# Kernel optimization log

Hardware: AMD Instinct MI355X
Metric: run time of the kernel (lower is better)

Reference implementation:

```python
import jax, jax.numpy as jnp
import numpy as np

EPS = 1e-5


def setup_inputs() -> dict:
    key = jax.random.key(0)
    ks = jax.random.split(key, 5)
    N, E, D, L = 10000, 160000, 512, 3
    x = jax.random.normal(ks[0], (N, D), dtype=jnp.float32)
    src = jax.random.randint(ks[1], (E,), 0, N, dtype=jnp.int64)
    dst = jax.random.randint(ks[2], (E,), 0, N, dtype=jnp.int64)
    gamma = jnp.ones((L, D), dtype=jnp.float32)
    beta = jnp.zeros((L, D), dtype=jnp.float32)
    # glorot-ish scale so ReLU stack stays well-conditioned
    W = jax.random.normal(ks[3], (L, D, D), dtype=jnp.float32) * (1.0 / np.sqrt(D))
    b = jnp.zeros((L, D), dtype=jnp.float32)
    return {"x": x, "src": src, "dst": dst, "gamma": gamma, "beta": beta, "W": W, "b": b}


def reference(x, src, dst, gamma, beta, W, b):
    N = x.shape[0]
    ones = jnp.ones(src.shape[0], dtype=x.dtype)
    # DGL GraphConv norm='both': src side uses out-degree, dst side uses in-degree
    out_deg = jnp.clip(jax.ops.segment_sum(ones, src, num_segments=N), 1.0)
    in_deg = jnp.clip(jax.ops.segment_sum(ones, dst, num_segments=N), 1.0)
    src_norm = (out_deg ** -0.5)[:, None]  # [N,1]
    dst_norm = (in_deg ** -0.5)[:, None]   # [N,1]
    n_layers = gamma.shape[0]
    for i in range(n_layers):
        # BatchNorm1d (training mode: batch mean, biased variance)
        mu = jnp.mean(x, axis=0)
        var = jnp.var(x, axis=0)
        x = (x - mu) * jax.lax.rsqrt(var + EPS) * gamma[i] + beta[i]
        h = x * src_norm
        agg = jax.ops.segment_sum(h[src], dst, num_segments=N) * dst_norm
        x = jax.nn.relu(agg @ W[i] + b[i])
    return x
```

## Files before the change

### kernel.cpp

```cpp
#include <hip/hip_runtime.h>
#include <hip/hip_bf16.h>

constexpr int N = 10000;
constexpr int D = 512;
constexpr int E = 160000;
constexpr int L = 3;
constexpr float EPS = 1e-5f;

typedef _Float16 half8 __attribute__((ext_vector_type(8)));
typedef _Float16 half2v __attribute__((ext_vector_type(2)));
typedef float floatx4 __attribute__((ext_vector_type(4)));

__device__ __forceinline__ void glds16(const _Float16* g, _Float16* l) {
    __builtin_amdgcn_global_load_lds(
        (const __attribute__((address_space(1))) uint32_t*)(g),
        (__attribute__((address_space(3))) uint32_t*)(l),
        16, 0, 0);
}

constexpr int DEG_BLOCKS  = (E + 255) / 256;
constexpr int CONV_BLOCKS = 100;
constexpr int TW_BLOCKS   = L * 256;
constexpr int MEGA_BLOCKS = DEG_BLOCKS + CONV_BLOCKS + TW_BLOCKS;

__global__ __launch_bounds__(256) void mega_setup(
    const int* __restrict__ src, const int* __restrict__ dst,
    const float* __restrict__ x, const float* __restrict__ W,
    int* __restrict__ out_deg, int* __restrict__ in_deg,
    _Float16* __restrict__ x16, float* __restrict__ stats0,
    _Float16* __restrict__ Wt) {
    __shared__ float tb[32][33];
    int bid = blockIdx.x;
    int tid = threadIdx.x;
    if (bid < DEG_BLOCKS) {
        int e = bid * 256 + tid;
        if (e < E) {
            atomicAdd(&out_deg[src[e]], 1);
            atomicAdd(&in_deg[dst[e]], 1);
        }
    } else if (bid < DEG_BLOCKS + CONV_BLOCKS) {
        int b = bid - DEG_BLOCKS;
        int r0 = b * 100;
        int r1 = r0 + 100; if (r1 > N) r1 = N;
        int c2 = tid * 2;
        float s0 = 0.f, s1 = 0.f, q0 = 0.f, q1 = 0.f;
        for (int r = r0; r < r1; ++r) {
            float2 v = *(const float2*)(x + (size_t)r * D + c2);
            s0 += v.x; q0 += v.x * v.x;
            s1 += v.y; q1 += v.y * v.y;
            half2v h; h[0] = (_Float16)v.x; h[1] = (_Float16)v.y;
            *(half2v*)(x16 + (size_t)r * D + c2) = h;
        }
        atomicAdd(&stats0[c2], s0);
        atomicAdd(&stats0[c2 + 1], s1);
        atomicAdd(&stats0[D + c2], q0);
        atomicAdd(&stats0[D + c2 + 1], q1);
    } else {
        int b = bid - DEG_BLOCKS - CONV_BLOCKS;
        int l = b >> 8;
        int t = b & 255;
        int k0 = (t >> 4) * 32, n0 = (t & 15) * 32;
        int tx = tid & 31, ty = tid >> 5;
        const float* Wl = W + (size_t)l * D * D;
        _Float16* Wtl = Wt + (size_t)l * D * D;
        for (int i = 0; i < 32; i += 8)
            tb[ty + i][tx] = Wl[(size_t)(k0 + ty + i) * D + n0 + tx];
        __syncthreads();
        for (int i = 0; i < 32; i += 8)
            Wtl[(size_t)(n0 + ty + i) * D + k0 + tx] = (_Float16)tb[tx][ty + i];
    }
}

__global__ void scan_indeg(const int* __restrict__ in_deg,
                           const int* __restrict__ out_deg,
                           int* __restrict__ off, int* __restrict__ cursor,
                           float* __restrict__ src_norm, float* __restrict__ dst_norm) {
    __shared__ int lsum[1024];
    int t = threadIdx.x;
    const int chunk = (N + 1023) / 1024;
    int start = t * chunk;
    int end = start + chunk; if (end > N) end = N;
    int s = 0;
    for (int i = start; i < end; ++i) s += in_deg[i];
    lsum[t] = s;
    __syncthreads();
    for (int d = 1; d < 1024; d <<= 1) {
        int v = (t >= d) ? lsum[t - d] : 0;
        __syncthreads();
        lsum[t] += v;
        __syncthreads();
    }
    int excl = (t == 0) ? 0 : lsum[t - 1];
    for (int i = start; i < end; ++i) {
        off[i] = excl;
        cursor[i] = excl;
        excl += in_deg[i];
        int od = out_deg[i]; if (od < 1) od = 1;
        int id = in_deg[i];  if (id < 1) id = 1;
        src_norm[i] = rsqrtf((float)od);
        dst_norm[i] = rsqrtf((float)id);
    }
    if (t == 1023) off[N] = lsum[1023];
}

__global__ void csr_fill(const int* __restrict__ src, const int* __restrict__ dst,
                         int* __restrict__ cursor, int* __restrict__ csr_src) {
    int e = blockIdx.x * blockDim.x + threadIdx.x;
    if (e >= E) return;
    int d = dst[e];
    int pos = atomicAdd(&cursor[d], 1);
    csr_src[pos] = src[e];
}

__global__ __launch_bounds__(256) void aggregate_bn(
    const _Float16* __restrict__ x, const int* __restrict__ off,
    const int* __restrict__ csr_src, const float* __restrict__ src_norm,
    const float* __restrict__ dst_norm, const float* __restrict__ stats,
    const float* __restrict__ gamma, const float* __restrict__ beta,
    _Float16* __restrict__ agg) {
    int wid = (blockIdx.x * 256 + threadIdx.x) >> 6;
    if (wid >= N) return;
    int lane = threadIdx.x & 63;
    int c0 = lane * 8;

    float scale[8], shift[8];
    const float invN = 1.0f / (float)N;
    for (int i = 0; i < 8; ++i) {
        int c = c0 + i;
        float mu = stats[c] * invN;
        float var = stats[D + c] * invN - mu * mu;
        float sc = gamma[c] * rsqrtf(var + EPS);
        scale[i] = sc;
        shift[i] = beta[c] - mu * sc;
    }

    int e0 = off[wid], e1 = off[wid + 1];
    float a[8] = {}, a2[8] = {};
    float t = 0.f;
    int e = e0;
    for (; e + 4 <= e1; e += 4) {
        int s0 = csr_src[e];
        int s1 = csr_src[e + 1];
        int s2 = csr_src[e + 2];
        int s3 = csr_src[e + 3];
        float n0 = src_norm[s0];
        float n1 = src_norm[s1];
        float n2 = src_norm[s2];
        float n3 = src_norm[s3];
        half8 v0 = *(const half8*)(x + (size_t)s0 * D + c0);
        half8 v1 = *(const half8*)(x + (size_t)s1 * D + c0);
        half8 v2 = *(const half8*)(x + (size_t)s2 * D + c0);
        half8 v3 = *(const half8*)(x + (size_t)s3 * D + c0);
        t += (n0 + n1) + (n2 + n3);
        for (int k = 0; k < 8; ++k) {
            a[k]  += (float)v0[k] * n0;
            a2[k] += (float)v1[k] * n1;
            a[k]  += (float)v2[k] * n2;
            a2[k] += (float)v3[k] * n3;
        }
    }
    for (; e < e1; ++e) {
        int s0 = csr_src[e];
        float n0 = src_norm[s0];
        half8 v0 = *(const half8*)(x + (size_t)s0 * D + c0);
        t += n0;
        for (int k = 0; k < 8; ++k) a[k] += (float)v0[k] * n0;
    }
    float dn = dst_norm[wid];
    half8 o;
    for (int i = 0; i < 8; ++i)
        o[i] = (_Float16)(dn * (scale[i] * (a[i] + a2[i]) + shift[i] * t));
    *(half8*)(agg + (size_t)wid * D + c0) = o;
}

template <typename OutT, bool STATS>
__global__ __launch_bounds__(256) void mm_f16_relu(
    const _Float16* __restrict__ A, const _Float16* __restrict__ Bt,
    const float* __restrict__ bias, OutT* __restrict__ C, int M,
    float* __restrict__ stats) {
    __shared__ __align__(16) _Float16 As[128 * 32];
    __shared__ __align__(16) _Float16 Bs[128 * 32];
    const int tid  = threadIdx.x;
    const int wave = tid >> 6;
    const int lane = tid & 63;
    const int quad = lane >> 4;
    const int l16  = lane & 15;
    const int row0 = blockIdx.x * 128;
    const int col0 = blockIdx.y * 128;
    const int wm = (wave & 1) * 64;
    const int wn = (wave >> 1) * 64;
    const int sr = lane >> 2;
    const int sc = (lane & 3) * 8;

    int ar0 = row0 + wave * 32 + sr;
    int ar1 = ar0 + 16;
    if (ar0 >= M) ar0 = M - 1;
    if (ar1 >= M) ar1 = M - 1;
    const _Float16* gA0 = A + (size_t)ar0 * D + sc;
    const _Float16* gA1 = A + (size_t)ar1 * D + sc;
    const _Float16* gB0 = Bt + (size_t)(col0 + wave * 32 + sr) * D + sc;
    const _Float16* gB1 = Bt + (size_t)(col0 + wave * 32 + 16 + sr) * D + sc;
    _Float16* lA0 = As + (wave * 32) * 32;
    _Float16* lA1 = As + (wave * 32 + 16) * 32;
    _Float16* lB0 = Bs + (wave * 32) * 32;
    _Float16* lB1 = Bs + (wave * 32 + 16) * 32;

    floatx4 acc[4][4] = {};

    for (int k0 = 0; k0 < D; k0 += 32) {
        __syncthreads();
        glds16(gA0 + k0, lA0);
        glds16(gA1 + k0, lA1);
        glds16(gB0 + k0, lB0);
        glds16(gB1 + k0, lB1);
        __syncthreads();
        half8 af[4], bf[4];
        for (int i = 0; i < 4; ++i)
            af[i] = *(const half8*)(As + (wm + i * 16 + l16) * 32 + quad * 8);
        for (int j = 0; j < 4; ++j)
            bf[j] = *(const half8*)(Bs + (wn + j * 16 + l16) * 32 + quad * 8);
        for (int i = 0; i < 4; ++i)
            for (int j = 0; j < 4; ++j)
                acc[i][j] = __builtin_amdgcn_mfma_f32_16x16x32_f16(
                    af[i], bf[j], acc[i][j], 0, 0, 0);
    }

    float s[4] = {}, q[4] = {};
    for (int i = 0; i < 4; ++i) {
        for (int r = 0; r < 4; ++r) {
            int row = row0 + wm + i * 16 + quad * 4 + r;
            bool valid = row < M;
            for (int j = 0; j < 4; ++j) {
                int col = col0 + wn + j * 16 + l16;
                float v = acc[i][j][r] + bias[col];
                v = v > 0.f ? v : 0.f;
                if (valid) {
                    C[(size_t)row * D + col] = (OutT)v;
                    if (STATS) { s[j] += v; q[j] += v * v; }
                }
            }
        }
    }
    if (STATS) {
        for (int j = 0; j < 4; ++j) {
            float sv = s[j], qv = q[j];
            sv += __shfl_xor(sv, 16); sv += __shfl_xor(sv, 32);
            qv += __shfl_xor(qv, 16); qv += __shfl_xor(qv, 32);
            if (quad == 0) {
                int col = col0 + wn + j * 16 + l16;
                atomicAdd(&stats[col], sv);
                atomicAdd(&stats[D + col], qv);
            }
        }
    }
}

extern "C" void kernel_launch(void* const* d_in, const int* in_sizes, int n_in,
                              void* d_out, int out_size, void* d_ws, size_t ws_size,
                              hipStream_t stream) {
    const float* x_in  = (const float*)d_in[0];
    const int*   src   = (const int*)d_in[1];
    const int*   dst   = (const int*)d_in[2];
    const float* gamma = (const float*)d_in[3];
    const float* beta  = (const float*)d_in[4];
    const float* W     = (const float*)d_in[5];
    const float* b     = (const float*)d_in[6];
    float* out = (float*)d_out;

    char* p = (char*)d_ws;
    _Float16* x16 = (_Float16*)p;  p += (size_t)N * D * 2;
    _Float16* agg = (_Float16*)p;  p += (size_t)N * D * 2;
    _Float16* Wt  = (_Float16*)p;  p += (size_t)L * D * D * 2;
    float* src_norm = (float*)p;   p += (size_t)N * 4;
    float* dst_norm = (float*)p;   p += (size_t)N * 4;
    int* out_deg   = (int*)p;      p += (size_t)N * 4;
    int* in_deg    = (int*)p;      p += (size_t)N * 4;
    float* stats0  = (float*)p;    p += 2 * D * 4;
    float* stats1  = (float*)p;    p += 2 * D * 4;
    float* stats2  = (float*)p;    p += 2 * D * 4;
    int* csr_off   = (int*)p;      p += (size_t)(N + 1) * 4;
    int* cursor    = (int*)p;      p += (size_t)N * 4;
    int* csr_src   = (int*)p;      p += (size_t)E * 4;

    float* stats_in[3] = {stats0, stats1, stats2};

    hipMemsetAsync(out_deg, 0, (2 * (size_t)N + 6 * D) * sizeof(int), stream);
    mega_setup<<<MEGA_BLOCKS, 256, 0, stream>>>(src, dst, x_in, W,
                                                out_deg, in_deg, x16, stats0, Wt);
    scan_indeg<<<1, 1024, 0, stream>>>(in_deg, out_deg, csr_off, cursor,
                                       src_norm, dst_norm);
    csr_fill<<<DEG_BLOCKS, 256, 0, stream>>>(src, dst, cursor, csr_src);

    dim3 mm_grid((N + 127) / 128, D / 128);
    const int agg_blocks = (N + 3) / 4;

    for (int l = 0; l < L; ++l) {
        const float* gl  = gamma + (size_t)l * D;
        const float* bl  = beta + (size_t)l * D;
        const _Float16* Wl = Wt + (size_t)l * D * D;
        const float* bil = b + (size_t)l * D;

        aggregate_bn<<<agg_blocks, 256, 0, stream>>>(
            x16, csr_off, csr_src, src_norm, dst_norm, stats_in[l], gl, bl, agg);
        if (l == L - 1) {
            mm_f16_relu<float, false><<<mm_grid, 256, 0, stream>>>(
                agg, Wl, bil, out, N, nullptr);
        } else {
            mm_f16_relu<_Float16, true><<<mm_grid, 256, 0, stream>>>(
                agg, Wl, bil, x16, N, stats_in[l + 1]);
        }
    }
}
```

Baseline: 282.3 us.

## Prescale features by src_norm, precompute per-dst norm sums, shard aggregation across column slices

Node features are now stored already multiplied by src_norm: the initial conversion does this in a new combined CSR-fill/convert kernel, and the GEMM epilogue does it for later layers. The per-destination sum of src_norm is accumulated once into T during CSR fill. This removes the per-edge src_norm gathers and multiplies from every layer's aggregation. Aggregation is split into 4 column shards per node, with four edge groups per wave reduced by shuffles, to raise parallelism and memory-level concurrency. The cost is extra atomics on T, more blocks, shuffle reductions, and an additional fp16 rounding of the prescaled values.

```diff
diff --git a/kernel.cpp b/kernel.cpp
--- a/kernel.cpp
+++ b/kernel.cpp
@@ -7,6 +7,9 @@
 constexpr int L = 3;
 constexpr float EPS = 1e-5f;
 
+constexpr int NSH = 4;
+constexpr int SHC = D / NSH;
+
 typedef _Float16 half8 __attribute__((ext_vector_type(8)));
 typedef _Float16 half2v __attribute__((ext_vector_type(2)));
 typedef float floatx4 __attribute__((ext_vector_type(4)));
@@ -19,16 +22,15 @@
 }
 
 constexpr int DEG_BLOCKS  = (E + 255) / 256;
-constexpr int CONV_BLOCKS = 100;
+constexpr int STAT_BLOCKS = 500;
 constexpr int TW_BLOCKS   = L * 256;
-constexpr int MEGA_BLOCKS = DEG_BLOCKS + CONV_BLOCKS + TW_BLOCKS;
+constexpr int MEGA_BLOCKS = DEG_BLOCKS + STAT_BLOCKS + TW_BLOCKS;
 
 __global__ __launch_bounds__(256) void mega_setup(
     const int* __restrict__ src, const int* __restrict__ dst,
     const float* __restrict__ x, const float* __restrict__ W,
     int* __restrict__ out_deg, int* __restrict__ in_deg,
-    _Float16* __restrict__ x16, float* __restrict__ stats0,
-    _Float16* __restrict__ Wt) {
+    float* __restrict__ stats0, _Float16* __restrict__ Wt) {
     __shared__ float tb[32][33];
     int bid = blockIdx.x;
     int tid = threadIdx.x;
@@ -38,25 +40,23 @@
             atomicAdd(&out_deg[src[e]], 1);
             atomicAdd(&in_deg[dst[e]], 1);
         }
-    } else if (bid < DEG_BLOCKS + CONV_BLOCKS) {
+    } else if (bid < DEG_BLOCKS + STAT_BLOCKS) {
         int b = bid - DEG_BLOCKS;
-        int r0 = b * 100;
-        int r1 = r0 + 100; if (r1 > N) r1 = N;
+        int r0 = b * 20;
+        int r1 = r0 + 20; if (r1 > N) r1 = N;
         int c2 = tid * 2;
         float s0 = 0.f, s1 = 0.f, q0 = 0.f, q1 = 0.f;
         for (int r = r0; r < r1; ++r) {
             float2 v = *(const float2*)(x + (size_t)r * D + c2);
             s0 += v.x; q0 += v.x * v.x;
             s1 += v.y; q1 += v.y * v.y;
-            half2v h; h[0] = (_Float16)v.x; h[1] = (_Float16)v.y;
-            *(half2v*)(x16 + (size_t)r * D + c2) = h;
         }
         atomicAdd(&stats0[c2], s0);
         atomicAdd(&stats0[c2 + 1], s1);
         atomicAdd(&stats0[D + c2], q0);
         atomicAdd(&stats0[D + c2 + 1], q1);
     } else {
-        int b = bid - DEG_BLOCKS - CONV_BLOCKS;
+        int b = bid - DEG_BLOCKS - STAT_BLOCKS;
         int l = b >> 8;
         int t = b & 255;
         int k0 = (t >> 4) * 32, n0 = (t & 15) * 32;
@@ -103,81 +103,98 @@
     if (t == 1023) off[N] = lsum[1023];
 }
 
-__global__ void csr_fill(const int* __restrict__ src, const int* __restrict__ dst,
-                         int* __restrict__ cursor, int* __restrict__ csr_src) {
-    int e = blockIdx.x * blockDim.x + threadIdx.x;
-    if (e >= E) return;
-    int d = dst[e];
-    int pos = atomicAdd(&cursor[d], 1);
-    csr_src[pos] = src[e];
-}
-
-__global__ __launch_bounds__(256) void aggregate_bn(
-    const _Float16* __restrict__ x, const int* __restrict__ off,
-    const int* __restrict__ csr_src, const float* __restrict__ src_norm,
+constexpr int CONV_BLOCKS = 500;
+__global__ __launch_bounds__(256) void csr_fill_conv(
+    const int* __restrict__ src, const int* __restrict__ dst,
+    const float* __restrict__ x, const float* __restrict__ src_norm,
+    int* __restrict__ cursor, int* __restrict__ csr_src,
+    float* __restrict__ T, _Float16* __restrict__ x16) {
+    int bid = blockIdx.x;
+    int tid = threadIdx.x;
+    if (bid < DEG_BLOCKS) {
+        int e = bid * 256 + tid;
+        if (e < E) {
+            int s = src[e], d = dst[e];
+            int pos = atomicAdd(&cursor[d], 1);
+            csr_src[pos] = s;
+            atomicAdd(&T[d], src_norm[s]);
+        }
+    } else {
+        int b = bid - DEG_BLOCKS;
+        int r0 = b * 20;
+        int r1 = r0 + 20; if (r1 > N) r1 = N;
+        int c2 = tid * 2;
+        for (int r = r0; r < r1; ++r) {
+            float sn = src_norm[r];
+            float2 v = *(const float2*)(x + (size_t)r * D + c2);
+            half2v h;
+            h[0] = (_Float16)(v.x * sn);
+            h[1] = (_Float16)(v.y * sn);
+            *(half2v*)(x16 + (size_t)r * D + c2) = h;
+        }
+    }
+}
+
+__global__ __launch_bounds__(256) void aggregate4(
+    const _Float16* __restrict__ xs, const int* __restrict__ off,
+    const int* __restrict__ csr_src, const float* __restrict__ T,
     const float* __restrict__ dst_norm, const float* __restrict__ stats,
     const float* __restrict__ gamma, const float* __restrict__ beta,
     _Float16* __restrict__ agg) {
-    int wid = (blockIdx.x * 256 + threadIdx.x) >> 6;
-    if (wid >= N) return;
+    int shard = blockIdx.x & 3;
+    int wid = (blockIdx.x >> 2) * 4 + (threadIdx.x >> 6);
     int lane = threadIdx.x & 63;
-    int c0 = lane * 8;
-
-    float scale[8], shift[8];
-    const float invN = 1.0f / (float)N;
-    for (int i = 0; i < 8; ++i) {
-        int c = c0 + i;
-        float mu = stats[c] * invN;
-        float var = stats[D + c] * invN - mu * mu;
-        float sc = gamma[c] * rsqrtf(var + EPS);
-        scale[i] = sc;
-        shift[i] = beta[c] - mu * sc;
-    }
+    int eg = lane >> 4;
+    int ch = lane & 15;
+    int c0 = shard * SHC + ch * 8;
 
     int e0 = off[wid], e1 = off[wid + 1];
-    float a[8] = {}, a2[8] = {};
-    float t = 0.f;
-    int e = e0;
-    for (; e + 4 <= e1; e += 4) {
+    const _Float16* xp = xs + c0;
+    float a[8] = {}, b2[8] = {};
+    int e = e0 + eg;
+    for (; e + 4 < e1; e += 8) {
         int s0 = csr_src[e];
-        int s1 = csr_src[e + 1];
-        int s2 = csr_src[e + 2];
-        int s3 = csr_src[e + 3];
-        float n0 = src_norm[s0];
-        float n1 = src_norm[s1];
-        float n2 = src_norm[s2];
-        float n3 = src_norm[s3];
-        half8 v0 = *(const half8*)(x + (size_t)s0 * D + c0);
-        half8 v1 = *(const half8*)(x + (size_t)s1 * D + c0);
-        half8 v2 = *(const half8*)(x + (size_t)s2 * D + c0);
-        half8 v3 = *(const half8*)(x + (size_t)s3 * D + c0);
-        t += (n0 + n1) + (n2 + n3);
+        int s1 = csr_src[e + 4];
+        half8 v0 = *(const half8*)(xp + (size_t)s0 * D);
+        half8 v1 = *(const half8*)(xp + (size_t)s1 * D);
+#pragma unroll
+        for (int k = 0; k < 8; ++k) { a[k] += (float)v0[k]; b2[k] += (float)v1[k]; }
+    }
+    if (e < e1) {
+        int s0 = csr_src[e];
+        half8 v0 = *(const half8*)(xp + (size_t)s0 * D);
+#pragma unroll
+        for (int k = 0; k < 8; ++k) a[k] += (float)v0[k];
+    }
+#pragma unroll
+    for (int k = 0; k < 8; ++k) {
+        a[k] += b2[k];
+        a[k] += __shfl_xor(a[k], 16);
+        a[k] += __shfl_xor(a[k], 32);
+    }
+    if (eg == 0) {
+        float t = T[wid];
+        float dn = dst_norm[wid];
+        const float invN = 1.0f / (float)N;
+        half8 o;
+#pragma unroll
         for (int k = 0; k < 8; ++k) {
-            a[k]  += (float)v0[k] * n0;
-            a2[k] += (float)v1[k] * n1;
-            a[k]  += (float)v2[k] * n2;
-            a2[k] += (float)v3[k] * n3;
-        }
-    }
-    for (; e < e1; ++e) {
-        int s0 = csr_src[e];
-        float n0 = src_norm[s0];
-        half8 v0 = *(const half8*)(x + (size_t)s0 * D + c0);
-        t += n0;
-        for (int k = 0; k < 8; ++k) a[k] += (float)v0[k] * n0;
-    }
-    float dn = dst_norm[wid];
-    half8 o;
-    for (int i = 0; i < 8; ++i)
-        o[i] = (_Float16)(dn * (scale[i] * (a[i] + a2[i]) + shift[i] * t));
-    *(half8*)(agg + (size_t)wid * D + c0) = o;
+            int c = c0 + k;
+            float mu = stats[c] * invN;
+            float var = stats[D + c] * invN - mu * mu;
+            float sc = gamma[c] * rsqrtf(var + EPS);
+            float sh = beta[c] - mu * sc;
+            o[k] = (_Float16)(dn * (sc * a[k] + sh * t));
+        }
+        *(half8*)(agg + (size_t)wid * D + c0) = o;
+    }
 }
 
 template <typename OutT, bool STATS>
 __global__ __launch_bounds__(256) void mm_f16_relu(
     const _Float16* __restrict__ A, const _Float16* __restrict__ Bt,
     const float* __restrict__ bias, OutT* __restrict__ C, int M,
-    float* __restrict__ stats) {
+    float* __restrict__ stats, const float* __restrict__ src_norm) {
     __shared__ __align__(16) _Float16 As[128 * 32];
     __shared__ __align__(16) _Float16 Bs[128 * 32];
     const int tid  = threadIdx.x;
@@ -230,13 +247,19 @@
         for (int r = 0; r < 4; ++r) {
             int row = row0 + wm + i * 16 + quad * 4 + r;
             bool valid = row < M;
+            float sn = 1.0f;
+            if (STATS && valid) sn = src_norm[row];
             for (int j = 0; j < 4; ++j) {
                 int col = col0 + wn + j * 16 + l16;
                 float v = acc[i][j][r] + bias[col];
                 v = v > 0.f ? v : 0.f;
                 if (valid) {
-                    C[(size_t)row * D + col] = (OutT)v;
-                    if (STATS) { s[j] += v; q[j] += v * v; }
+                    if (STATS) {
+                        C[(size_t)row * D + col] = (OutT)(v * sn);
+                        s[j] += v; q[j] += v * v;
+                    } else {
+                        C[(size_t)row * D + col] = (OutT)v;
+                    }
                 }
             }
         }
@@ -278,21 +301,23 @@
     float* stats0  = (float*)p;    p += 2 * D * 4;
     float* stats1  = (float*)p;    p += 2 * D * 4;
     float* stats2  = (float*)p;    p += 2 * D * 4;
+    float* T       = (float*)p;    p += (size_t)N * 4;
     int* csr_off   = (int*)p;      p += (size_t)(N + 1) * 4;
     int* cursor    = (int*)p;      p += (size_t)N * 4;
     int* csr_src   = (int*)p;      p += (size_t)E * 4;
 
     float* stats_in[3] = {stats0, stats1, stats2};
 
-    hipMemsetAsync(out_deg, 0, (2 * (size_t)N + 6 * D) * sizeof(int), stream);
+    hipMemsetAsync(out_deg, 0, (3 * (size_t)N + 6 * D) * sizeof(int), stream);
     mega_setup<<<MEGA_BLOCKS, 256, 0, stream>>>(src, dst, x_in, W,
-                                                out_deg, in_deg, x16, stats0, Wt);
+                                                out_deg, in_deg, stats0, Wt);
     scan_indeg<<<1, 1024, 0, stream>>>(in_deg, out_deg, csr_off, cursor,
                                        src_norm, dst_norm);
-    csr_fill<<<DEG_BLOCKS, 256, 0, stream>>>(src, dst, cursor, csr_src);
+    csr_fill_conv<<<DEG_BLOCKS + CONV_BLOCKS, 256, 0, stream>>>(
+        src, dst, x_in, src_norm, cursor, csr_src, T, x16);
 
     dim3 mm_grid((N + 127) / 128, D / 128);
-    const int agg_blocks = (N + 3) / 4;
+    const int agg_blocks = NSH * ((N + 3) / 4);
 
     for (int l = 0; l < L; ++l) {
         const float* gl  = gamma + (size_t)l * D;
@@ -300,14 +325,14 @@
         const _Float16* Wl = Wt + (size_t)l * D * D;
         const float* bil = b + (size_t)l * D;
 
-        aggregate_bn<<<agg_blocks, 256, 0, stream>>>(
-            x16, csr_off, csr_src, src_norm, dst_norm, stats_in[l], gl, bl, agg);
+        aggregate4<<<agg_blocks, 256, 0, stream>>>(
+            x16, csr_off, csr_src, T, dst_norm, stats_in[l], gl, bl, agg);
         if (l == L - 1) {
             mm_f16_relu<float, false><<<mm_grid, 256, 0, stream>>>(
-                agg, Wl, bil, out, N, nullptr);
+                agg, Wl, bil, out, N, nullptr, nullptr);
         } else {
             mm_f16_relu<_Float16, true><<<mm_grid, 256, 0, stream>>>(
-                agg, Wl, bil, x16, N, stats_in[l + 1]);
-        }
-    }
-}
+                agg, Wl, bil, x16, N, stats_in[l + 1], src_norm);
+        }
+    }
+}
```

New measurement: 321.1 us. 13.7% more time.
